# Performance work log

Measured on AMD Instinct MI355X. Metric: run time of the kernel, lower is better.

The kernel has to match this reference:

```python
import jax, jax.numpy as jnp
import numpy as np
from jax import lax

HEAD_DIM = 32
SCALE = HEAD_DIM ** -0.5
BN_EPS = 1e-5


def _bn_relu(x, g, b):
    # training-mode BatchNorm2d over (B,H,W) per channel, biased variance, then ReLU
    mean = jnp.mean(x, axis=(0, 1, 2))
    var = jnp.var(x, axis=(0, 1, 2))
    y = (x - mean) * lax.rsqrt(var + BN_EPS) * g + b
    return jax.nn.relu(y)


def _pool2x2(y, op):
    # AvgPool2d/MaxPool2d(kernel=2, stride=2) on [B,pH,pW,C]
    B, pH, pW, C = y.shape
    y = y.reshape(B, pH // 2, 2, pW // 2, 2, C)
    return op(y, axis=(2, 4))


def setup_inputs() -> dict:
    key = jax.random.key(0)
    ks = jax.random.split(key, 12)
    B, H, W, C, pC = 16, 32, 32, 512, 256
    s = lambda k, shape, fan: jax.random.normal(k, shape, jnp.float32) * (fan ** -0.5)
    return {
        "x": jax.random.normal(ks[0], (B, H, W, C), jnp.float32),
        "prevx": jax.random.normal(ks[1], (B, 2 * H, 2 * W, pC), jnp.float32),
        "w_prev_qkv": s(ks[2], (C, pC), pC),          # Linear(prev_dim->dim), no bias
        "w_qkv": s(ks[3], (C, C), C),                  # Linear(dim->dim), no bias
        "fuse_w": s(ks[4], (2 * C, C), 2 * C),         # 1x1 conv as [Cin, Cout]
        "fuse_b": jax.random.normal(ks[5], (C,), jnp.float32) * 0.01,
        "bn1_g": jnp.ones((C,), jnp.float32) + jax.random.normal(ks[6], (C,), jnp.float32) * 0.01,
        "bn1_b": jax.random.normal(ks[7], (C,), jnp.float32) * 0.01,
        "out_w": s(ks[8], (3, 3, C, C), 9 * C),        # 3x3 conv HWIO
        "out_b": jax.random.normal(ks[9], (C,), jnp.float32) * 0.01,
        "bn2_g": jnp.ones((C,), jnp.float32) + jax.random.normal(ks[10], (C,), jnp.float32) * 0.01,
        "bn2_b": jax.random.normal(ks[11], (C,), jnp.float32) * 0.01,
        "gamma": jnp.array([0.3], jnp.float32),
        "beta": jnp.array([0.4], jnp.float32),
    }


def reference(x, prevx, w_prev_qkv, w_qkv, fuse_w, fuse_b, bn1_g, bn1_b,
              out_w, out_b, bn2_g, bn2_b, gamma, beta):
    B, H, W, C = x.shape
    N = H * W

    prevqkv = prevx @ w_prev_qkv.T                       # [B,2H,2W,C]
    qkv = (x @ w_qkv.T).reshape(B, N, C)                 # [B,N,C]
    avg_kv = _pool2x2(prevqkv, jnp.mean).reshape(B, -1, C)
    max_kv = _pool2x2(prevqkv, jnp.max).reshape(B, -1, C)

    def attn(q, k, v):
        a = jax.nn.softmax(jnp.einsum('bnc,bmc->bnm', q, k) * SCALE, axis=-1)
        o = jnp.einsum('bnm,bmc->bnc', a, v)
        # faithful to torch: (attn@v).transpose(1,2).reshape(B,H,W,-1)
        return jnp.swapaxes(o, 1, 2).reshape(B, H, W, C)

    x_now = attn(qkv, qkv, qkv)
    avgx_prev = attn(qkv, avg_kv, avg_kv)
    maxx_prev = attn(qkv, max_kv, max_kv)
    x_prev = beta[0] * avgx_prev + (1.0 - beta[0]) * maxx_prev

    cat = jnp.concatenate([x_now, x_prev], axis=-1)      # [B,H,W,2C]
    fusx = _bn_relu(jnp.einsum('bhwi,io->bhwo', cat, fuse_w) + fuse_b, bn1_g, bn1_b)
    x = x + gamma[0] * fusx

    y = lax.conv_general_dilated(x, out_w, window_strides=(1, 1), padding='SAME',
                                 dimension_numbers=('NHWC', 'HWIO', 'NHWC')) + out_b
    return _bn_relu(y, bn2_g, bn2_b)
```

## Files before the change

kernel.cpp:

```cpp
#include <hip/hip_runtime.h>
#include <hip/hip_bf16.h>

#define B_   16
#define C_   512
#define N_   1024
#define NTOK 16384
#define SCALE_ 0.17677669529663687f
#define EPS_ 1e-5f

typedef __attribute__((ext_vector_type(8))) short bf16x8;
typedef __attribute__((ext_vector_type(4))) float f32x4;
typedef __attribute__((ext_vector_type(4))) short sh4;

#define GLOBAL_AS __attribute__((address_space(1)))
#define LDS_AS    __attribute__((address_space(3)))
#define MFMA16 __builtin_amdgcn_mfma_f32_16x16x32_bf16

__device__ __forceinline__ short f2bs(float v){
    __hip_bfloat16 h = __float2bfloat16(v);
    return *reinterpret_cast<short*>(&h);
}
__device__ __forceinline__ float bs2f(short s){
    __hip_bfloat16 h = *reinterpret_cast<__hip_bfloat16*>(&s);
    return __bfloat162float(h);
}
__device__ __forceinline__ void gload16(const void* g, void* l){
    __builtin_amdgcn_global_load_lds((const GLOBAL_AS unsigned int*)g,
                                     (LDS_AS unsigned int*)l, 16, 0, 0);
}

enum { AG_ROW = 0, AG_POOL = 1, AG_FUSE = 2, AG_CONV = 3, AG_SEL3 = 4, AG_QK = 5 };
enum { EP_QKV = 0, EP_POOL = 1, EP_PVN = 7, EP_FUSE_STATS = 8, EP_SPLIT_F32 = 9, EP_SCOREP = 10 };
enum { ORD_INNER_N = 0, ORD_INNER_M = 1 };

__global__ __launch_bounds__(256) void k_zero(float* p, int n){
    int i = blockIdx.x*256 + threadIdx.x;
    if (i < n) p[i] = 0.f;
}

__global__ __launch_bounds__(256) void k_cast(const float* __restrict__ s, short* __restrict__ d, int n){
    int i = (blockIdx.x*256 + threadIdx.x)*4;
    if (i >= n) return;
    float4 v = *reinterpret_cast<const float4*>(s + i);
    sh4 o; o[0]=f2bs(v.x); o[1]=f2bs(v.y); o[2]=f2bs(v.z); o[3]=f2bs(v.w);
    *reinterpret_cast<sh4*>(d + i) = o;
}

__global__ __launch_bounds__(256) void k_tcast(const float* __restrict__ src, short* __restrict__ dst,
                                               int R, int Cc){
    __shared__ float t[32][33];
    int bx = blockIdx.x*32, by = blockIdx.y*32;
    int tx = threadIdx.x & 31, ty = threadIdx.x >> 5;
    #pragma unroll
    for (int i = 0; i < 32; i += 8)
        t[ty+i][tx] = src[(size_t)(by+ty+i)*Cc + bx+tx];
    __syncthreads();
    #pragma unroll
    for (int i = 0; i < 32; i += 8)
        dst[(size_t)(bx+ty+i)*R + by+tx] = f2bs(t[tx][ty+i]);
}

template<int AM, int EP, int ORDER, int NX, int NY, int NZ, int NT, int KT, int KROW, int KSPLIT,
         long ASTR, long BSTR>
__global__ __launch_bounds__(256) void k_mm(const short* __restrict__ A,
                                            const short* __restrict__ Bt,
                                            const short* __restrict__ A2,
                                            const float* __restrict__ sc0,
                                            void* __restrict__ O0,
                                            void* __restrict__ O1,
                                            void* __restrict__ O2,
                                            void* __restrict__ O3){
    __shared__ short Asm[128*32];
    __shared__ short Bsm[128*32];
    const int tid = threadIdx.x, wave = tid >> 6, lane = tid & 63;

    constexpr int nwg = NX*NY*NZ;
    constexpr int q8 = nwg >> 3, r8 = nwg & 7;
    int orig = blockIdx.x;
    int xcd = orig & 7, idx8 = orig >> 3;
    int wg = (xcd < r8 ? xcd*(q8+1) : r8*(q8+1) + (xcd - r8)*q8) + idx8;
    int bz = wg / (NX*NY);
    int rem = wg - bz*(NX*NY);
    int nx, my;
    if constexpr (ORDER == ORD_INNER_N){ my = rem / NX; nx = rem - my*NX; }
    else                               { nx = rem / NY; my = rem - nx*NY; }

    const int m0 = my*128, n0 = nx*128;
    const short* Ab;
    if constexpr (AM == AG_SEL3){
        const short* base = (bz < 16) ? A : (bz < 32) ? A2 : (const short*)O3;
        Ab = base + (size_t)(bz & 15)*ASTR;
    } else if constexpr (AM == AG_QK){
        Ab = A + (size_t)(bz & 15)*ASTR;
    } else {
        Ab = A + (size_t)bz*ASTR;
    }
    const short* Bb;
    if constexpr (AM == AG_QK){
        const short* bbase = (bz < 16) ? Bt : (bz < 32) ? A2 : (const short*)O3;
        Bb = bbase + (size_t)(bz & 15)*BSTR;
    } else {
        Bb = Bt + (size_t)bz*BSTR;
    }

    f32x4 acc[4][4];
    #pragma unroll
    for (int i = 0; i < 4; ++i)
        #pragma unroll
        for (int j = 0; j < 4; ++j)
            acc[i][j] = (f32x4){0.f,0.f,0.f,0.f};

    const int wm = (wave >> 1)*64, wn = (wave & 1)*64;
    const int lrow = lane & 15, lk = (lane >> 4)*8;

    for (int k0 = 0; k0 < KT; k0 += 32){
        #pragma unroll
        for (int is = 0; is < 2; ++is){
            int fl = is*256 + tid;
            int r = fl >> 2, ccol = (fl & 3)*8;
            int kk = bz*KSPLIT + k0 + ccol;
            const short* ga;
            if constexpr (AM == AG_ROW || AM == AG_SEL3 || AM == AG_QK){
                ga = Ab + (size_t)(m0 + r)*KROW + kk;
            } else if constexpr (AM == AG_POOL){
                int m = m0 + r;
                int b = m >> 12, rem2 = m & 4095, g = rem2 >> 2, qd = rem2 & 3;
                int srow = (b*64 + (g>>5)*2 + (qd>>1))*64 + (g&31)*2 + (qd&1);
                ga = Ab + (size_t)srow*KROW + kk;
            } else if constexpr (AM == AG_FUSE){
                int m = m0 + r;
                int b = m >> 10, rem2 = m & 1023, h = rem2 >> 5, w = rem2 & 31;
                const short* src = (kk < 512) ? A : A2;
                ga = src + ((size_t)(b*512 + h*16 + (w>>1))*1024 + ((w&1)<<9) + (kk & 511));
            } else {
                int m = m0 + r;
                int b = m >> 10, rem2 = m & 1023, h = rem2 >> 5, w = rem2 & 31;
                int tap = kk >> 9, ic = kk & 511;
                int dh = tap/3 - 1, dw = tap - (tap/3)*3 - 1;
                int hs = h + dh, wd = w + dw;
                if (hs >= 0 && hs < 32 && wd >= 0 && wd < 32)
                    ga = A + ((size_t)((b*32 + hs)*32 + wd)*512 + ic);
                else
                    ga = A2;
            }
            gload16(ga, &Asm[(is*4 + wave)*512]);
            const short* gb = Bb + (size_t)(n0 + r)*KROW + kk;
            gload16(gb, &Bsm[(is*4 + wave)*512]);
        }
        __syncthreads();
        bf16x8 af[4], bfr[4];
        #pragma unroll
        for (int mi = 0; mi < 4; ++mi)
            af[mi] = *(const bf16x8*)&Asm[(wm + mi*16 + lrow)*32 + lk];
        #pragma unroll
        for (int nj = 0; nj < 4; ++nj)
            bfr[nj] = *(const bf16x8*)&Bsm[(wn + nj*16 + lrow)*32 + lk];
        #pragma unroll
        for (int mi = 0; mi < 4; ++mi)
            #pragma unroll
            for (int nj = 0; nj < 4; ++nj)
                acc[mi][nj] = MFMA16(af[mi], bfr[nj], acc[mi][nj], 0, 0, 0);
        __syncthreads();
    }

    const int lg = lane >> 4;

    if constexpr (EP == EP_FUSE_STATS){
        float* redS = (float*)Asm;
        float* redQ = (float*)Bsm;
        #pragma unroll
        for (int nj = 0; nj < 4; ++nj){
            int c = n0 + wn + nj*16 + lrow;
            float bias = sc0[c];
            float s = 0.f, qq = 0.f;
            #pragma unroll
            for (int mi = 0; mi < 4; ++mi){
                int r0 = m0 + wm + mi*16 + lg*4;
                #pragma unroll
                for (int rg = 0; rg < 4; ++rg){
                    float val = acc[mi][nj][rg] + bias;
                    s += val; qq += val*val;
                    ((short*)O0)[(size_t)(r0+rg)*NT + c] = f2bs(val);
                }
            }
            int chl = wn + nj*16 + lrow;
            int slot = (wave >> 1)*4 + lg;
            redS[chl*8 + slot] = s;
            redQ[chl*8 + slot] = qq;
        }
        __syncthreads();
        if (tid < 128){
            float S = 0.f, Q = 0.f;
            #pragma unroll
            for (int k = 0; k < 8; ++k){ S += redS[tid*8 + k]; Q += redQ[tid*8 + k]; }
            atomicAdd(&((float*)O1)[n0 + tid], S);
            atomicAdd(&((float*)O2)[n0 + tid], Q);
        }
        return;
    }

    if constexpr (EP == EP_SCOREP){
        short* Pb = (short*)O0 + ((size_t)bz << 20);
        float* lsum = (float*)O1 + (size_t)bz*1024;
        #pragma unroll
        for (int mi = 0; mi < 4; ++mi){
            int r0 = m0 + wm + mi*16 + lg*4;
            float s4[4] = {0.f, 0.f, 0.f, 0.f};
            #pragma unroll
            for (int nj = 0; nj < 4; ++nj){
                int c = n0 + wn + nj*16 + lrow;
                f32x4 v = acc[mi][nj];
                #pragma unroll
                for (int rg = 0; rg < 4; ++rg){
                    float p = __expf(fminf(v[rg]*SCALE_, 80.f));
                    s4[rg] += p;
                    Pb[(size_t)(r0+rg)*NT + c] = f2bs(p);
                }
            }
            #pragma unroll
            for (int off = 1; off < 16; off <<= 1){
                #pragma unroll
                for (int rg = 0; rg < 4; ++rg) s4[rg] += __shfl_xor(s4[rg], off);
            }
            if (lrow == 0){
                #pragma unroll
                for (int rg = 0; rg < 4; ++rg) atomicAdd(&lsum[r0+rg], s4[rg]);
            }
        }
        return;
    }

    #pragma unroll
    for (int mi = 0; mi < 4; ++mi)
        #pragma unroll
        for (int nj = 0; nj < 4; ++nj){
            int c  = n0 + wn + nj*16 + lrow;
            int r0 = m0 + wm + mi*16 + lg*4;
            f32x4 v = acc[mi][nj];
            if constexpr (EP == EP_QKV){
                sh4 t4;
                #pragma unroll
                for (int rg = 0; rg < 4; ++rg){
                    short s = f2bs(v[rg]);
                    ((short*)O0)[(size_t)(r0+rg)*NT + c] = s;
                    t4[rg] = s;
                }
                int b = r0 >> 10, t = r0 & 1023;
                *reinterpret_cast<sh4*>((short*)O1 + ((size_t)(b*512 + c))*1024 + t) = t4;
            } else if constexpr (EP == EP_POOL){
                float av = 0.25f*(v[0]+v[1]+v[2]+v[3]);
                float mx = fmaxf(fmaxf(v[0],v[1]), fmaxf(v[2],v[3]));
                int g = r0 >> 2;
                int b = g >> 10, t = g & 1023;
                ((short*)O0)[(size_t)g*512 + c] = f2bs(av);
                ((short*)O2)[(size_t)g*512 + c] = f2bs(mx);
                ((short*)O1)[((size_t)(b*512 + c))*1024 + t] = f2bs(av);
                ((short*)O3)[((size_t)(b*512 + c))*1024 + t] = f2bs(mx);
            } else if constexpr (EP == EP_PVN){
                short* Ob = ((bz < 16) ? (short*)O0 : (bz < 32) ? (short*)O1 : (short*)O2)
                            + (size_t)(bz & 15)*524288;
                float sc = 1.f / sc0[(size_t)bz*1024 + c];
                #pragma unroll
                for (int rg = 0; rg < 4; ++rg)
                    Ob[(size_t)(r0+rg)*NT + c] = f2bs(v[rg]*sc);
            } else {
                float* O = (float*)O0 + (size_t)bz*((long)NTOK*NT);
                #pragma unroll
                for (int rg = 0; rg < 4; ++rg)
                    O[(size_t)(r0+rg)*NT + c] = v[rg];
            }
        }
}

__global__ __launch_bounds__(256) void k_combine(const short* __restrict__ av,
                                                 const short* __restrict__ mx,
                                                 short* __restrict__ o,
                                                 const float* __restrict__ beta){
    int i = (blockIdx.x*256 + threadIdx.x)*8;
    float be = beta[0];
    bf16x8 va = *(const bf16x8*)&av[i];
    bf16x8 vm = *(const bf16x8*)&mx[i];
    bf16x8 vo;
    #pragma unroll
    for (int j = 0; j < 8; ++j)
        vo[j] = f2bs(be*bs2f(va[j]) + (1.f - be)*bs2f(vm[j]));
    *reinterpret_cast<bf16x8*>(&o[i]) = vo;
}

__global__ __launch_bounds__(256) void k_stats2(const float* __restrict__ p0,
                                                const float* __restrict__ p1,
                                                const float* __restrict__ bias,
                                                float* __restrict__ Y,
                                                float* __restrict__ sum, float* __restrict__ sumsq){
    int t = threadIdx.x, c0 = t*2, r0 = blockIdx.x*32;
    float b0 = bias[c0], b1 = bias[c0+1];
    float s0=0, s1=0, q0=0, q1=0;
    for (int r = 0; r < 32; ++r){
        size_t off = (size_t)(r0+r)*C_ + c0;
        float2 a = *reinterpret_cast<const float2*>(p0 + off);
        float2 b = *reinterpret_cast<const float2*>(p1 + off);
        float v0 = a.x + b.x + b0, v1 = a.y + b.y + b1;
        float2 ov; ov.x = v0; ov.y = v1;
        *reinterpret_cast<float2*>(Y + off) = ov;
        s0 += v0; q0 += v0*v0; s1 += v1; q1 += v1*v1;
    }
    atomicAdd(&sum[c0],   s0); atomicAdd(&sum[c0+1],   s1);
    atomicAdd(&sumsq[c0], q0); atomicAdd(&sumsq[c0+1], q1);
}

__global__ __launch_bounds__(256) void k_apply1(const short* __restrict__ fusxq,
                                                const float* __restrict__ x,
                                                const float* __restrict__ sum,
                                                const float* __restrict__ sumsq,
                                                const float* __restrict__ g,
                                                const float* __restrict__ bb,
                                                const float* __restrict__ gamma,
                                                short* __restrict__ x2q){
    int i4 = (blockIdx.x*256 + threadIdx.x)*4;
    int c = i4 & (C_-1);
    sh4 f = *reinterpret_cast<const sh4*>(fusxq + i4);
    float4 xv = *reinterpret_cast<const float4*>(x + i4);
    float gm = gamma[0];
    sh4 o;
    #pragma unroll
    for (int j = 0; j < 4; ++j){
        int cj = c + j;
        float mean = sum[cj]*(1.f/NTOK);
        float var  = sumsq[cj]*(1.f/NTOK) - mean*mean;
        float t = (bs2f(f[j]) - mean)*rsqrtf(var + EPS_)*g[cj] + bb[cj];
        float xj = (j==0) ? xv.x : (j==1) ? xv.y : (j==2) ? xv.z : xv.w;
        o[j] = f2bs(xj + gm*fmaxf(t, 0.f));
    }
    *reinterpret_cast<sh4*>(x2q + i4) = o;
}

__global__ __launch_bounds__(256) void k_apply2(float* __restrict__ Y,
                                                const float* __restrict__ sum,
                                                const float* __restrict__ sumsq,
                                                const float* __restrict__ g,
                                                const float* __restrict__ bb){
    int i4 = (blockIdx.x*256 + threadIdx.x)*4;
    int c = i4 & (C_-1);
    float4 v = *reinterpret_cast<float4*>(Y + i4);
    float o[4] = {v.x, v.y, v.z, v.w};
    #pragma unroll
    for (int j = 0; j < 4; ++j){
        int cj = c + j;
        float mean = sum[cj]*(1.f/NTOK);
        float var  = sumsq[cj]*(1.f/NTOK) - mean*mean;
        float t = (o[j] - mean)*rsqrtf(var + EPS_)*g[cj] + bb[cj];
        o[j] = fmaxf(t, 0.f);
    }
    float4 ov; ov.x = o[0]; ov.y = o[1]; ov.z = o[2]; ov.w = o[3];
    *reinterpret_cast<float4*>(Y + i4) = ov;
}

extern "C" void kernel_launch(void* const* d_in, const int* in_sizes, int n_in,
                              void* d_out, int out_size, void* d_ws, size_t ws_size,
                              hipStream_t stream){
    const float* x      = (const float*)d_in[0];
    const float* prevx  = (const float*)d_in[1];
    const float* w_prev = (const float*)d_in[2];
    const float* w_qkv  = (const float*)d_in[3];
    const float* fuse_w = (const float*)d_in[4];
    const float* fuse_b = (const float*)d_in[5];
    const float* bn1_g  = (const float*)d_in[6];
    const float* bn1_b  = (const float*)d_in[7];
    const float* out_w  = (const float*)d_in[8];
    const float* out_b  = (const float*)d_in[9];
    const float* bn2_g  = (const float*)d_in[10];
    const float* bn2_b  = (const float*)d_in[11];
    const float* gamma  = (const float*)d_in[12];
    const float* beta   = (const float*)d_in[13];
    float* out = (float*)d_out;

    char* ws8 = (char*)d_ws;
    short* pxq  = (short*)(ws8 + 0);
    short* xq   = (short*)(ws8 + 33554432);
    short* Pall = (short*)(ws8 + 0);
    float* cpart= (float*)(ws8 + 0);
    short* qkvT = (short*)(ws8 + 100663296);
    short* x2q  = (short*)(ws8 + 100663296);
    short* avgkT= (short*)(ws8 + 117440512);
    short* maxkT= (short*)(ws8 + 134217728);
    short* prevT= maxkT;
    short* nowT = (short*)(ws8 + 150994944);
    short* avgk = nowT;
    short* avgT = (short*)(ws8 + 167772160);
    short* maxk = avgT;
    short* maxT = (short*)(ws8 + 184549376);
    short* fusxq= (short*)(ws8 + 184549376);
    short* qkv  = (short*)(ws8 + 201326592);
    short* wqT  = (short*)(ws8 + 218103808);
    short* wpT  = (short*)(ws8 + 218628096);
    short* wfT  = (short*)(ws8 + 218890240);
    short* wcT  = (short*)(ws8 + 219938816);
    float* st   = (float*)(ws8 + 224657408);
    short* zpg  = (short*)(ws8 + 224665600);
    float* lsum = (float*)(ws8 + 224666624);
    float *s1sum = st, *s1sq = st + 512, *s2sum = st + 1024, *s2sq = st + 1536;

    dim3 blk(256);
    k_zero<<<9, blk, 0, stream>>>(st, 2304);
    k_zero<<<192, blk, 0, stream>>>(lsum, 49152);
    k_cast<<<8192, blk, 0, stream>>>(x, xq, 8388608);
    k_cast<<<256,  blk, 0, stream>>>(w_qkv, wqT, 262144);
    k_cast<<<128,  blk, 0, stream>>>(w_prev, wpT, 131072);
    k_tcast<<<dim3(16, 32),  blk, 0, stream>>>(fuse_w, wfT, 1024, 512);
    k_tcast<<<dim3(16, 144), blk, 0, stream>>>(out_w, wcT, 4608, 512);
    k_cast<<<16384, blk, 0, stream>>>(prevx, pxq, 16777216);

    k_mm<AG_ROW, EP_QKV, ORD_INNER_N, 4, 128, 1, 512, 512, 512, 0, 0L, 0L>
        <<<512, blk, 0, stream>>>(xq, wqT, nullptr, nullptr,
                                  qkv, qkvT, nullptr, nullptr);
    k_mm<AG_POOL, EP_POOL, ORD_INNER_N, 4, 512, 1, 512, 256, 256, 0, 0L, 0L>
        <<<2048, blk, 0, stream>>>(pxq, wpT, nullptr, nullptr,
                                   avgk, avgkT, maxk, maxkT);
    k_mm<AG_QK, EP_SCOREP, ORD_INNER_M, 8, 8, 48, 1024, 512, 512, 0, 524288L, 524288L>
        <<<3072, blk, 0, stream>>>(qkv, qkv, avgk, nullptr,
                                   Pall, lsum, nullptr, maxk);
    k_mm<AG_SEL3, EP_PVN, ORD_INNER_M, 8, 4, 48, 1024, 1024, 1024, 0, 524288L, 1048576L>
        <<<1536, blk, 0, stream>>>(qkvT, Pall, avgkT, lsum,
                                   nowT, avgT, maxT, maxkT);
    k_combine<<<4096, blk, 0, stream>>>(avgT, maxT, prevT, beta);
    k_mm<AG_FUSE, EP_FUSE_STATS, ORD_INNER_N, 4, 128, 1, 512, 1024, 1024, 0, 0L, 0L>
        <<<512, blk, 0, stream>>>(nowT, wfT, prevT, fuse_b,
                                  fusxq, s1sum, s1sq, nullptr);
    k_apply1<<<8192, blk, 0, stream>>>(fusxq, x, s1sum, s1sq, bn1_g, bn1_b, gamma, x2q);
    k_mm<AG_CONV, EP_SPLIT_F32, ORD_INNER_N, 4, 128, 2, 512, 2304, 4608, 2304, 0L, 0L>
        <<<1024, blk, 0, stream>>>(x2q, wcT, zpg, nullptr,
                                   cpart, nullptr, nullptr, nullptr);
    k_stats2<<<512, blk, 0, stream>>>(cpart, cpart + (size_t)NTOK*C_, out_b, out, s2sum, s2sq);
    k_apply2<<<8192, blk, 0, stream>>>(out, s2sum, s2sq, bn2_g, bn2_b);
}
```

Baseline: 474.4 us.

## Fuse fp32-to-bf16 input casts into QKV and pooled-projection GEMM loads

The QKV and prev-QKV GEMMs now load fp32 activations straight into a doubled LDS A tile and convert them to bf16 while building MFMA fragments, so the separate cast kernels for x and prevx and their bf16 intermediate buffers are gone. This removes a full extra read and write pass over the two largest inputs, in exchange for twice the A-tile load traffic per k-step, larger LDS use and conversion work in the inner loop. The two zeroing launches are merged into one, and the conv stats kernel is rewritten to use float4 accesses across two row halves.

```diff
diff --git a/kernel.cpp b/kernel.cpp
--- a/kernel.cpp
+++ b/kernel.cpp
@@ -29,7 +29,8 @@
                                      (LDS_AS unsigned int*)l, 16, 0, 0);
 }
 
-enum { AG_ROW = 0, AG_POOL = 1, AG_FUSE = 2, AG_CONV = 3, AG_SEL3 = 4, AG_QK = 5 };
+enum { AG_ROW = 0, AG_POOL = 1, AG_FUSE = 2, AG_CONV = 3, AG_SEL3 = 4, AG_QK = 5,
+       AG_ROWF = 6, AG_POOLF = 7 };
 enum { EP_QKV = 0, EP_POOL = 1, EP_PVN = 7, EP_FUSE_STATS = 8, EP_SPLIT_F32 = 9, EP_SCOREP = 10 };
 enum { ORD_INNER_N = 0, ORD_INNER_M = 1 };
 
@@ -70,7 +71,8 @@
                                             void* __restrict__ O1,
                                             void* __restrict__ O2,
                                             void* __restrict__ O3){
-    __shared__ short Asm[128*32];
+    constexpr bool AF32 = (AM == AG_ROWF || AM == AG_POOLF);
+    __shared__ short Asm[AF32 ? 128*64 : 128*32];
     __shared__ short Bsm[128*32];
     const int tid = threadIdx.x, wave = tid >> 6, lane = tid & 63;
 
@@ -114,44 +116,84 @@
     const int lrow = lane & 15, lk = (lane >> 4)*8;
 
     for (int k0 = 0; k0 < KT; k0 += 32){
-        #pragma unroll
-        for (int is = 0; is < 2; ++is){
-            int fl = is*256 + tid;
-            int r = fl >> 2, ccol = (fl & 3)*8;
-            int kk = bz*KSPLIT + k0 + ccol;
-            const short* ga;
-            if constexpr (AM == AG_ROW || AM == AG_SEL3 || AM == AG_QK){
-                ga = Ab + (size_t)(m0 + r)*KROW + kk;
-            } else if constexpr (AM == AG_POOL){
-                int m = m0 + r;
-                int b = m >> 12, rem2 = m & 4095, g = rem2 >> 2, qd = rem2 & 3;
-                int srow = (b*64 + (g>>5)*2 + (qd>>1))*64 + (g&31)*2 + (qd&1);
-                ga = Ab + (size_t)srow*KROW + kk;
-            } else if constexpr (AM == AG_FUSE){
-                int m = m0 + r;
-                int b = m >> 10, rem2 = m & 1023, h = rem2 >> 5, w = rem2 & 31;
-                const short* src = (kk < 512) ? A : A2;
-                ga = src + ((size_t)(b*512 + h*16 + (w>>1))*1024 + ((w&1)<<9) + (kk & 511));
-            } else {
-                int m = m0 + r;
-                int b = m >> 10, rem2 = m & 1023, h = rem2 >> 5, w = rem2 & 31;
-                int tap = kk >> 9, ic = kk & 511;
-                int dh = tap/3 - 1, dw = tap - (tap/3)*3 - 1;
-                int hs = h + dh, wd = w + dw;
-                if (hs >= 0 && hs < 32 && wd >= 0 && wd < 32)
-                    ga = A + ((size_t)((b*32 + hs)*32 + wd)*512 + ic);
-                else
-                    ga = A2;
-            }
-            gload16(ga, &Asm[(is*4 + wave)*512]);
-            const short* gb = Bb + (size_t)(n0 + r)*KROW + kk;
-            gload16(gb, &Bsm[(is*4 + wave)*512]);
+        if constexpr (AF32){
+            const float* Afp = (const float*)A;
+            #pragma unroll
+            for (int is = 0; is < 4; ++is){
+                int fl = is*256 + tid;
+                int r = fl >> 3, c4 = (fl & 7)*4;
+                const float* gaf;
+                if constexpr (AM == AG_ROWF){
+                    gaf = Afp + (size_t)(m0 + r)*KROW + k0 + c4;
+                } else {
+                    int m = m0 + r;
+                    int b = m >> 12, rem2 = m & 4095, g = rem2 >> 2, qd = rem2 & 3;
+                    int srow = (b*64 + (g>>5)*2 + (qd>>1))*64 + (g&31)*2 + (qd&1);
+                    gaf = Afp + (size_t)srow*KROW + k0 + c4;
+                }
+                gload16(gaf, &Asm[(is*256 + wave*64)*8]);
+            }
+            #pragma unroll
+            for (int is = 0; is < 2; ++is){
+                int fl = is*256 + tid;
+                int r = fl >> 2, ccol = (fl & 3)*8;
+                const short* gb = Bb + (size_t)(n0 + r)*KROW + k0 + ccol;
+                gload16(gb, &Bsm[(is*4 + wave)*512]);
+            }
+        } else {
+            #pragma unroll
+            for (int is = 0; is < 2; ++is){
+                int fl = is*256 + tid;
+                int r = fl >> 2, ccol = (fl & 3)*8;
+                int kk = bz*KSPLIT + k0 + ccol;
+                const short* ga;
+                if constexpr (AM == AG_ROW || AM == AG_SEL3 || AM == AG_QK){
+                    ga = Ab + (size_t)(m0 + r)*KROW + kk;
+                } else if constexpr (AM == AG_POOL){
+                    int m = m0 + r;
+                    int b = m >> 12, rem2 = m & 4095, g = rem2 >> 2, qd = rem2 & 3;
+                    int srow = (b*64 + (g>>5)*2 + (qd>>1))*64 + (g&31)*2 + (qd&1);
+                    ga = Ab + (size_t)srow*KROW + kk;
+                } else if constexpr (AM == AG_FUSE){
+                    int m = m0 + r;
+                    int b = m >> 10, rem2 = m & 1023, h = rem2 >> 5, w = rem2 & 31;
+                    const short* src = (kk < 512) ? A : A2;
+                    ga = src + ((size_t)(b*512 + h*16 + (w>>1))*1024 + ((w&1)<<9) + (kk & 511));
+                } else {
+                    int m = m0 + r;
+                    int b = m >> 10, rem2 = m & 1023, h = rem2 >> 5, w = rem2 & 31;
+                    int tap = kk >> 9, ic = kk & 511;
+                    int dh = tap/3 - 1, dw = tap - (tap/3)*3 - 1;
+                    int hs = h + dh, wd = w + dw;
+                    if (hs >= 0 && hs < 32 && wd >= 0 && wd < 32)
+                        ga = A + ((size_t)((b*32 + hs)*32 + wd)*512 + ic);
+                    else
+                        ga = A2;
+                }
+                gload16(ga, &Asm[(is*4 + wave)*512]);
+                const short* gb = Bb + (size_t)(n0 + r)*KROW + kk;
+                gload16(gb, &Bsm[(is*4 + wave)*512]);
+            }
         }
         __syncthreads();
         bf16x8 af[4], bfr[4];
-        #pragma unroll
-        for (int mi = 0; mi < 4; ++mi)
-            af[mi] = *(const bf16x8*)&Asm[(wm + mi*16 + lrow)*32 + lk];
+        if constexpr (AF32){
+            const float* Afl = (const float*)Asm;
+            #pragma unroll
+            for (int mi = 0; mi < 4; ++mi){
+                int rr = wm + mi*16 + lrow;
+                float4 u0 = *(const float4*)&Afl[rr*32 + lk];
+                float4 u1 = *(const float4*)&Afl[rr*32 + lk + 4];
+                bf16x8 a;
+                a[0]=f2bs(u0.x); a[1]=f2bs(u0.y); a[2]=f2bs(u0.z); a[3]=f2bs(u0.w);
+                a[4]=f2bs(u1.x); a[5]=f2bs(u1.y); a[6]=f2bs(u1.z); a[7]=f2bs(u1.w);
+                af[mi] = a;
+            }
+        } else {
+            #pragma unroll
+            for (int mi = 0; mi < 4; ++mi)
+                af[mi] = *(const bf16x8*)&Asm[(wm + mi*16 + lrow)*32 + lk];
+        }
         #pragma unroll
         for (int nj = 0; nj < 4; ++nj)
             bfr[nj] = *(const bf16x8*)&Bsm[(wn + nj*16 + lrow)*32 + lk];
@@ -292,20 +334,27 @@
                                                 const float* __restrict__ bias,
                                                 float* __restrict__ Y,
                                                 float* __restrict__ sum, float* __restrict__ sumsq){
-    int t = threadIdx.x, c0 = t*2, r0 = blockIdx.x*32;
-    float b0 = bias[c0], b1 = bias[c0+1];
-    float s0=0, s1=0, q0=0, q1=0;
-    for (int r = 0; r < 32; ++r){
-        size_t off = (size_t)(r0+r)*C_ + c0;
-        float2 a = *reinterpret_cast<const float2*>(p0 + off);
-        float2 b = *reinterpret_cast<const float2*>(p1 + off);
-        float v0 = a.x + b.x + b0, v1 = a.y + b.y + b1;
-        float2 ov; ov.x = v0; ov.y = v1;
-        *reinterpret_cast<float2*>(Y + off) = ov;
-        s0 += v0; q0 += v0*v0; s1 += v1; q1 += v1*v1;
-    }
-    atomicAdd(&sum[c0],   s0); atomicAdd(&sum[c0+1],   s1);
-    atomicAdd(&sumsq[c0], q0); atomicAdd(&sumsq[c0+1], q1);
+    int t = threadIdx.x;
+    int c0 = (t & 127)*4;
+    int r0 = blockIdx.x*32 + (t >> 7)*16;
+    float4 bz4 = *reinterpret_cast<const float4*>(bias + c0);
+    float s[4] = {0,0,0,0}, q[4] = {0,0,0,0};
+    for (int r = 0; r < 16; ++r){
+        size_t off = (size_t)(r0 + r)*C_ + c0;
+        float4 a = *reinterpret_cast<const float4*>(p0 + off);
+        float4 b = *reinterpret_cast<const float4*>(p1 + off);
+        float v0 = a.x + b.x + bz4.x, v1 = a.y + b.y + bz4.y;
+        float v2 = a.z + b.z + bz4.z, v3 = a.w + b.w + bz4.w;
+        float4 ov = make_float4(v0, v1, v2, v3);
+        *reinterpret_cast<float4*>(Y + off) = ov;
+        s[0]+=v0; q[0]+=v0*v0; s[1]+=v1; q[1]+=v1*v1;
+        s[2]+=v2; q[2]+=v2*v2; s[3]+=v3; q[3]+=v3*v3;
+    }
+    #pragma unroll
+    for (int j = 0; j < 4; ++j){
+        atomicAdd(&sum[c0+j],   s[j]);
+        atomicAdd(&sumsq[c0+j], q[j]);
+    }
 }
 
 __global__ __launch_bounds__(256) void k_apply1(const short* __restrict__ fusxq,
@@ -375,8 +424,6 @@
     float* out = (float*)d_out;
 
     char* ws8 = (char*)d_ws;
-    short* pxq  = (short*)(ws8 + 0);
-    short* xq   = (short*)(ws8 + 33554432);
     short* Pall = (short*)(ws8 + 0);
     float* cpart= (float*)(ws8 + 0);
     short* qkvT = (short*)(ws8 + 100663296);
@@ -401,20 +448,17 @@
     float *s1sum = st, *s1sq = st + 512, *s2sum = st + 1024, *s2sq = st + 1536;
 
     dim3 blk(256);
-    k_zero<<<9, blk, 0, stream>>>(st, 2304);
-    k_zero<<<192, blk, 0, stream>>>(lsum, 49152);
-    k_cast<<<8192, blk, 0, stream>>>(x, xq, 8388608);
+    k_zero<<<201, blk, 0, stream>>>(st, 51456);
     k_cast<<<256,  blk, 0, stream>>>(w_qkv, wqT, 262144);
     k_cast<<<128,  blk, 0, stream>>>(w_prev, wpT, 131072);
     k_tcast<<<dim3(16, 32),  blk, 0, stream>>>(fuse_w, wfT, 1024, 512);
     k_tcast<<<dim3(16, 144), blk, 0, stream>>>(out_w, wcT, 4608, 512);
-    k_cast<<<16384, blk, 0, stream>>>(prevx, pxq, 16777216);
-
-    k_mm<AG_ROW, EP_QKV, ORD_INNER_N, 4, 128, 1, 512, 512, 512, 0, 0L, 0L>
-        <<<512, blk, 0, stream>>>(xq, wqT, nullptr, nullptr,
+
+    k_mm<AG_ROWF, EP_QKV, ORD_INNER_N, 4, 128, 1, 512, 512, 512, 0, 0L, 0L>
+        <<<512, blk, 0, stream>>>((const short*)x, wqT, nullptr, nullptr,
                                   qkv, qkvT, nullptr, nullptr);
-    k_mm<AG_POOL, EP_POOL, ORD_INNER_N, 4, 512, 1, 512, 256, 256, 0, 0L, 0L>
-        <<<2048, blk, 0, stream>>>(pxq, wpT, nullptr, nullptr,
+    k_mm<AG_POOLF, EP_POOL, ORD_INNER_N, 4, 512, 1, 512, 256, 256, 0, 0L, 0L>
+        <<<2048, blk, 0, stream>>>((const short*)prevx, wpT, nullptr, nullptr,
                                    avgk, avgkT, maxk, maxkT);
     k_mm<AG_QK, EP_SCOREP, ORD_INNER_M, 8, 8, 48, 1024, 512, 512, 0, 524288L, 524288L>
         <<<3072, blk, 0, stream>>>(qkv, qkv, avgk, nullptr,
```

New measurement: 629.7 us. 32.7% more time.
